# Performance work log

Measured on AMD Instinct MI355X. Metric: run time of the kernel, lower is better.

Reference implementation:

```python
import jax, jax.numpy as jnp
import numpy as np

DIM = 512        # model dim
MOE_DIM = 256    # expert hidden dim
E = 64           # n_routed experts
G = 8            # n_routed_group
TOPK_G = 4       # n_topk_group
K = 8            # n_experts_per_tok
SCALE = 2.5      # routed_scale
CAP = 1024


def setup_inputs() -> dict:
    key = jax.random.key(0)
    ks = jax.random.split(key, 6)
    x = jax.random.normal(ks[0], (4, 512, DIM), jnp.float32)
    gate_w = jax.random.normal(ks[1], (E, DIM), jnp.float32) / np.sqrt(DIM).astype(np.float32)
    gate_b = jax.random.normal(ks[2], (E,), jnp.float32) * 0.01
    w1 = jax.random.normal(ks[3], (E, DIM, MOE_DIM), jnp.float32) / np.sqrt(DIM).astype(np.float32)
    w3 = jax.random.normal(ks[4], (E, DIM, MOE_DIM), jnp.float32) / np.sqrt(DIM).astype(np.float32)
    w2 = jax.random.normal(ks[5], (E, MOE_DIM, DIM), jnp.float32) / np.sqrt(MOE_DIM).astype(np.float32)
    return {"x": x, "gate_w": gate_w, "gate_b": gate_b, "w1": w1, "w3": w3, "w2": w2}


def _gate(x2, gate_w, gate_b):
    # x2: [T, DIM] -> (weights [T,K], indices [T,K])
    T = x2.shape[0]
    scores = jax.nn.sigmoid(x2 @ gate_w.T)                      # [T, E]
    s = (scores + gate_b).reshape(T, G, E // G)                  # grouped scores
    group_scores = jax.lax.top_k(s, 2)[0].sum(-1)                # [T, G] sum of top-2 per group
    top_groups = jax.lax.top_k(group_scores, TOPK_G)[1]          # [T, TOPK_G]
    gmask = jnp.zeros((T, G), bool).at[jnp.arange(T)[:, None], top_groups].set(True)
    s = jnp.where(gmask[..., None], s, -jnp.inf).reshape(T, E)
    idx = jax.lax.top_k(s, K)[1]                                 # [T, K]
    w = jnp.take_along_axis(scores, idx, axis=1)                 # original (pre-bias) scores
    w = w / w.sum(-1, keepdims=True) * SCALE
    return w, idx


def _moe_forward(x, gate_w, gate_b, w1, w3, w2):
    shape = x.shape
    x2 = x.reshape(-1, DIM)                                      # [T, DIM]
    T = x2.shape[0]
    w, idx = _gate(x2, gate_w, gate_b)
    flat_e = idx.reshape(-1)                                     # [T*K]
    # position of each (token, slot) within its expert's buffer, in order
    oh = (flat_e[:, None] == jnp.arange(E)[None, :]).astype(jnp.int32)  # [T*K, E]
    pos = (jnp.cumsum(oh, axis=0) * oh).sum(-1) - 1              # [T*K]
    x_rep = jnp.repeat(x2, K, axis=0)                            # [T*K, DIM]
    # dispatch into per-expert buffers [E, CAP, DIM]
    xb = jnp.zeros((E, CAP, DIM), x2.dtype).at[flat_e, pos].set(x_rep, mode='drop')
    h = jax.nn.silu(jnp.einsum('ecd,edm->ecm', xb, w1)) * jnp.einsum('ecd,edm->ecm', xb, w3)
    yb = jnp.einsum('ecm,emd->ecd', h, w2)                       # [E, CAP, DIM]
    # combine: gather back and weight
    y = yb.at[flat_e, pos].get(mode='fill', fill_value=0.0) * w.reshape(-1)[:, None]
    return y.reshape(T, K, DIM).sum(1).reshape(shape)


def reference(x, gate_w, gate_b, w1, w3, w2):
    return _moe_forward(x, gate_w, gate_b, w1, w3, w2)
```

## Files before the change

### kernel.cpp

```cpp
#include <hip/hip_runtime.h>

#define T_TOK 2048
#define DIM   512
#define MOE   256
#define NE    64
#define NG    8
#define TOPKG 4
#define TOPK  8
#define CAP   1024
#define MOE_SCALE 2.5f

typedef float f32x4 __attribute__((ext_vector_type(4)));
typedef short s16x8 __attribute__((ext_vector_type(8)));

__device__ __forceinline__ unsigned short f2bf(float f) {
    unsigned u = __builtin_bit_cast(unsigned, f);
    unsigned r = (u + 0x7fffu + ((u >> 16) & 1u)) >> 16;
    return (unsigned short)r;
}
__device__ __forceinline__ unsigned pk2(float lo, float hi) {
    return (unsigned)f2bf(lo) | ((unsigned)f2bf(hi) << 16);
}

__device__ __forceinline__ void tile_scan(const int* __restrict__ counts, int lane,
                                          int e, int& G0, int& ne, int& nt)
{
    int cl = min(counts[lane], CAP);
    int ntl = (cl + 31) >> 5;
    int v = ntl;
#pragma unroll
    for (int d = 1; d < 64; d <<= 1) {
        int o = __shfl_up(v, d);
        if (lane >= d) v += o;
    }
    G0 = __shfl(v - ntl, e);
    ne = __shfl(cl, e);
    nt = __shfl(ntl, e);
}

__global__ __launch_bounds__(256) void gwt_k(const float* __restrict__ gw,
                                             float* __restrict__ gwT)
{
    int idx = blockIdx.x * 256 + threadIdx.x;
    int e = idx >> 9, k = idx & 511;
    gwT[(size_t)(k >> 2) * 256 + e * 4 + (k & 3)] = gw[idx];
}

__global__ __launch_bounds__(256) void gate_fused_k(const float* __restrict__ x,
                                                    const float* __restrict__ gwT,
                                                    const float* __restrict__ gb,
                                                    int* __restrict__ counts,
                                                    int* __restrict__ etok,
                                                    float* __restrict__ wt_of,
                                                    short* __restrict__ xb)
{
    __shared__ float xs[4][512];
    __shared__ float ps[4][4][64];
    int w = threadIdx.x >> 6, lane = threadIdx.x & 63;
    int t = blockIdx.x * 4 + w;

    {
        const float4* xr = (const float4*)(x + (size_t)t * DIM);
        float4 v0 = xr[lane * 2], v1 = xr[lane * 2 + 1];
        *(float4*)&xs[w][lane * 8]     = v0;
        *(float4*)&xs[w][lane * 8 + 4] = v1;
        short o[8];
        o[0] = (short)f2bf(v0.x); o[1] = (short)f2bf(v0.y);
        o[2] = (short)f2bf(v0.z); o[3] = (short)f2bf(v0.w);
        o[4] = (short)f2bf(v1.x); o[5] = (short)f2bf(v1.y);
        o[6] = (short)f2bf(v1.z); o[7] = (short)f2bf(v1.w);
        *(s16x8*)(xb + (size_t)t * DIM + lane * 8) = *(const s16x8*)o;
    }
    __syncthreads();

    const f32x4* gt = (const f32x4*)gwT;
    float a0 = 0.f, a1 = 0.f, a2 = 0.f, a3 = 0.f;
    int kb = w * 32;
#pragma unroll 8
    for (int k4 = 0; k4 < 32; ++k4) {
        f32x4 g  = gt[(size_t)(kb + k4) * 64 + lane];
        f32x4 x0 = *(const f32x4*)&xs[0][(kb + k4) * 4];
        f32x4 x1 = *(const f32x4*)&xs[1][(kb + k4) * 4];
        f32x4 x2 = *(const f32x4*)&xs[2][(kb + k4) * 4];
        f32x4 x3 = *(const f32x4*)&xs[3][(kb + k4) * 4];
        a0 += g.x * x0.x + g.y * x0.y + g.z * x0.z + g.w * x0.w;
        a1 += g.x * x1.x + g.y * x1.y + g.z * x1.z + g.w * x1.w;
        a2 += g.x * x2.x + g.y * x2.y + g.z * x2.z + g.w * x2.w;
        a3 += g.x * x3.x + g.y * x3.y + g.z * x3.z + g.w * x3.w;
    }
    ps[w][0][lane] = a0; ps[w][1][lane] = a1;
    ps[w][2][lane] = a2; ps[w][3][lane] = a3;
    __syncthreads();
    float acc = ps[0][w][lane] + ps[1][w][lane] + ps[2][w][lane] + ps[3][w][lane];

    float sc = 1.f / (1.f + __expf(-acc));
    float s  = sc + gb[lane];

    float m1 = s, m2 = -1e30f;
#pragma unroll
    for (int d = 1; d < 8; d <<= 1) {
        float o1 = __shfl_xor(m1, d);
        float o2 = __shfl_xor(m2, d);
        float n1 = fmaxf(m1, o1);
        float n2 = fmaxf(fminf(m1, o1), fmaxf(m2, o2));
        m1 = n1; m2 = n2;
    }
    float gv = m1 + m2;

    bool gkeep = false;
#pragma unroll
    for (int it = 0; it < TOPKG; ++it) {
        float m = gv;
#pragma unroll
        for (int d = 1; d < 64; d <<= 1) m = fmaxf(m, __shfl_xor(m, d));
        unsigned long long mask = __ballot(gv == m);
        int ldr = __ffsll(mask) - 1;
        if ((lane >> 3) == (ldr >> 3)) { gkeep = true; gv = -2e30f; }
    }
    float sv = gkeep ? s : -1e30f;

    float wsum = 0.f;
    int my_e = 0; float my_w = 0.f;
#pragma unroll
    for (int k = 0; k < TOPK; ++k) {
        float m = sv;
#pragma unroll
        for (int d = 1; d < 64; d <<= 1) m = fmaxf(m, __shfl_xor(m, d));
        unsigned long long mask = __ballot(sv == m);
        int l = __ffsll(mask) - 1;
        float wk = __shfl(sc, l);
        wsum += wk;
        if (lane == k) { my_e = l; my_w = wk; }
        if (lane == l) sv = -2e30f;
    }
    float scale = MOE_SCALE / wsum;
    if (lane < TOPK) {
        int p = atomicAdd(&counts[my_e], 1);
        int rid = t * TOPK + lane;
        bool ok = (p < CAP);
        if (ok) etok[my_e * CAP + p] = rid;
        wt_of[rid] = ok ? my_w * scale : 0.f;
    }
}

__global__ __launch_bounds__(256) void dispatch_k(const short* __restrict__ xb,
                                                  const int* __restrict__ counts,
                                                  const int* __restrict__ etok,
                                                  short* __restrict__ xg)
{
    int e = blockIdx.x & 63, sub = blockIdx.x >> 6;
    int w = threadIdx.x >> 6, lane = threadIdx.x & 63;

    int G0, ne, nt;
    tile_scan(counts, lane, e, G0, ne, nt);
    int rows = nt * 32;
    const int* el = etok + e * CAP;

    int kt = lane >> 2, qq = lane & 3;
    for (int p = sub * 4 + w; p < rows; p += 32) {
        s16x8 v = {0, 0, 0, 0, 0, 0, 0, 0};
        if (p < ne) {
            int tok = el[p] >> 3;
            v = *(const s16x8*)(xb + (size_t)tok * DIM + lane * 8);
        }
        int st = (p >> 4) & 1, m = p & 15;
        size_t off = ((((size_t)(G0 + (p >> 5)) * 16 + kt) * 2 + st) * 64
                      + (qq * 16 + m)) * 8;
        *(s16x8*)(xg + off) = v;
    }
}

__global__ __launch_bounds__(256, 2) void gemm1_k(const short* __restrict__ xg,
                                                  const float* __restrict__ w1,
                                                  const float* __restrict__ w3,
                                                  const int* __restrict__ counts,
                                                  short* __restrict__ hgf)
{
    __shared__ short Bl[2][16][2][64][8];
    __shared__ short Ct[4][2][16][24];

    int e  = blockIdx.x & 63, cg = blockIdx.x >> 6;
    int n0 = cg * 32;
    int tid = threadIdx.x;
    int w = tid >> 6, lane = tid & 63;
    int q = lane >> 4, m16 = lane & 15;

    int G0, ne, nt;
    tile_scan(counts, lane, e, G0, ne, nt);

    const float* W1e = w1 + (size_t)e * DIM * MOE + n0;
    const float* W3e = w3 + (size_t)e * DIM * MOE + n0;
#pragma unroll 4
    for (int it = 0; it < 16; ++it) {
        int idx = it * 256 + tid;
        int mat = idx >> 11;
        int rem = idx & 2047;
        int r2  = rem >> 3;
        int cq  = (rem & 7) * 4;
        int k   = r2 * 2;
        int kt = k >> 5, qf = (k >> 3) & 3, j0 = k & 7;
        int cgrp = cq >> 4, c15 = cq & 15;
        const float* p = (mat ? W3e : W1e) + (size_t)k * MOE + cq;
        f32x4 lo = __builtin_nontemporal_load((const f32x4*)p);
        f32x4 hi = __builtin_nontemporal_load((const f32x4*)(p + MOE));
        unsigned* b = (unsigned*)&Bl[mat][kt][cgrp][qf * 16 + c15][j0];
        b[0]  = pk2(lo.x, hi.x);
        b[4]  = pk2(lo.y, hi.y);
        b[8]  = pk2(lo.z, hi.z);
        b[12] = pk2(lo.w, hi.w);
    }
    __syncthreads();

    for (int T = w; T < nt; T += 4) {
        const short* A = xg + (size_t)(G0 + T) * 16384 + lane * 8;

        f32x4 acc[2][2][2];
#pragma unroll
        for (int i = 0; i < 2; ++i)
#pragma unroll
            for (int j = 0; j < 2; ++j)
#pragma unroll
                for (int c = 0; c < 2; ++c) acc[i][j][c] = (f32x4)0.f;

        s16x8 pa0[4], pa1[4];
#pragma unroll
        for (int i = 0; i < 4; ++i) {
            pa0[i] = *(const s16x8*)(A + (i * 2 + 0) * 512);
            pa1[i] = *(const s16x8*)(A + (i * 2 + 1) * 512);
        }
#pragma unroll
        for (int kt = 0; kt < 16; ++kt) {
            s16x8 a0 = pa0[kt & 3], a1 = pa1[kt & 3];
            if (kt < 12) {
                pa0[kt & 3] = *(const s16x8*)(A + ((kt + 4) * 2 + 0) * 512);
                pa1[kt & 3] = *(const s16x8*)(A + ((kt + 4) * 2 + 1) * 512);
            }
            s16x8 b10 = *(const s16x8*)&Bl[0][kt][0][lane][0];
            s16x8 b11 = *(const s16x8*)&Bl[0][kt][1][lane][0];
            s16x8 b30 = *(const s16x8*)&Bl[1][kt][0][lane][0];
            s16x8 b31 = *(const s16x8*)&Bl[1][kt][1][lane][0];
            acc[0][0][0] = __builtin_amdgcn_mfma_f32_16x16x32_bf16(a0, b10, acc[0][0][0], 0, 0, 0);
            acc[1][0][0] = __builtin_amdgcn_mfma_f32_16x16x32_bf16(a1, b10, acc[1][0][0], 0, 0, 0);
            acc[0][0][1] = __builtin_amdgcn_mfma_f32_16x16x32_bf16(a0, b11, acc[0][0][1], 0, 0, 0);
            acc[1][0][1] = __builtin_amdgcn_mfma_f32_16x16x32_bf16(a1, b11, acc[1][0][1], 0, 0, 0);
            acc[0][1][0] = __builtin_amdgcn_mfma_f32_16x16x32_bf16(a0, b30, acc[0][1][0], 0, 0, 0);
            acc[1][1][0] = __builtin_amdgcn_mfma_f32_16x16x32_bf16(a1, b30, acc[1][1][0], 0, 0, 0);
            acc[0][1][1] = __builtin_amdgcn_mfma_f32_16x16x32_bf16(a0, b31, acc[0][1][1], 0, 0, 0);
            acc[1][1][1] = __builtin_amdgcn_mfma_f32_16x16x32_bf16(a1, b31, acc[1][1][1], 0, 0, 0);
        }

#pragma unroll
        for (int cgrp = 0; cgrp < 2; ++cgrp) {
#pragma unroll
            for (int sub = 0; sub < 2; ++sub)
#pragma unroll
                for (int r = 0; r < 4; ++r) {
                    float g = acc[sub][0][cgrp][r];
                    float u = acc[sub][1][cgrp][r];
                    float hv = g / (1.f + __expf(-g)) * u;
                    Ct[w][sub][q * 4 + r][m16] = (short)f2bf(hv);
                }
            int subr = q >> 1;
            s16x8 hv8 = *(const s16x8*)&Ct[w][subr][m16][(q & 1) * 8];
            size_t slot = ((size_t)(G0 + T) * 8 + cg) * 2 + subr;
            *(s16x8*)(hgf + slot * 512 + (cgrp * 2 + (q & 1)) * 128 + m16 * 8) = hv8;
        }
    }
}

__global__ __launch_bounds__(256, 2) void gemm2_k(const short* __restrict__ hgf,
                                                  const float* __restrict__ w2,
                                                  const int* __restrict__ counts,
                                                  const int* __restrict__ etok,
                                                  short* __restrict__ ybuf)
{
    __shared__ short Bl[4][8][64][8];

    int e  = blockIdx.x & 63, cg = blockIdx.x >> 6;
    int n0 = cg * 64;
    int tid = threadIdx.x;
    int w = tid >> 6, lane = tid & 63;
    int q = lane >> 4, m16 = lane & 15;

    int G0, ne, nt;
    tile_scan(counts, lane, e, G0, ne, nt);

    const float* W2e = w2 + (size_t)e * MOE * DIM + n0;
#pragma unroll 4
    for (int it = 0; it < 8; ++it) {
        int idx = it * 256 + tid;
        int r2  = idx >> 4;
        int cq  = (idx & 15) * 4;
        int k   = r2 * 2;
        int kt2 = k >> 5, qf = (k >> 3) & 3, j0 = k & 7;
        int s = cq >> 4, c15 = cq & 15;
        const float* p = W2e + (size_t)k * DIM + cq;
        f32x4 lo = __builtin_nontemporal_load((const f32x4*)p);
        f32x4 hi = __builtin_nontemporal_load((const f32x4*)(p + DIM));
        unsigned* b = (unsigned*)&Bl[s][kt2][qf * 16 + c15][j0];
        b[0]  = pk2(lo.x, hi.x);
        b[4]  = pk2(lo.y, hi.y);
        b[8]  = pk2(lo.z, hi.z);
        b[12] = pk2(lo.w, hi.w);
    }
    __syncthreads();

    const int* el = etok + e * CAP;

    for (int T = w; T < nt; T += 4) {
        const short* A = hgf + (size_t)(G0 + T) * 8192 + lane * 8;

        int erid[2][4];
#pragma unroll
        for (int sub = 0; sub < 2; ++sub)
#pragma unroll
            for (int r = 0; r < 4; ++r) {
                int row = T * 32 + sub * 16 + q * 4 + r;
                erid[sub][r] = row < ne ? el[row] : -1;
            }

        f32x4 acc[2][4];
#pragma unroll
        for (int i = 0; i < 2; ++i)
#pragma unroll
            for (int j = 0; j < 4; ++j) acc[i][j] = (f32x4)0.f;

        s16x8 pa0[4], pa1[4];
#pragma unroll
        for (int i = 0; i < 4; ++i) {
            pa0[i] = *(const s16x8*)(A + (i * 2 + 0) * 512);
            pa1[i] = *(const s16x8*)(A + (i * 2 + 1) * 512);
        }
#pragma unroll
        for (int kt = 0; kt < 8; ++kt) {
            s16x8 a0 = pa0[kt & 3], a1 = pa1[kt & 3];
            if (kt < 4) {
                pa0[kt & 3] = *(const s16x8*)(A + ((kt + 4) * 2 + 0) * 512);
                pa1[kt & 3] = *(const s16x8*)(A + ((kt + 4) * 2 + 1) * 512);
            }
            s16x8 b0 = *(const s16x8*)&Bl[0][kt][lane][0];
            s16x8 b1 = *(const s16x8*)&Bl[1][kt][lane][0];
            s16x8 b2 = *(const s16x8*)&Bl[2][kt][lane][0];
            s16x8 b3 = *(const s16x8*)&Bl[3][kt][lane][0];
            acc[0][0] = __builtin_amdgcn_mfma_f32_16x16x32_bf16(a0, b0, acc[0][0], 0, 0, 0);
            acc[1][0] = __builtin_amdgcn_mfma_f32_16x16x32_bf16(a1, b0, acc[1][0], 0, 0, 0);
            acc[0][1] = __builtin_amdgcn_mfma_f32_16x16x32_bf16(a0, b1, acc[0][1], 0, 0, 0);
            acc[1][1] = __builtin_amdgcn_mfma_f32_16x16x32_bf16(a1, b1, acc[1][1], 0, 0, 0);
            acc[0][2] = __builtin_amdgcn_mfma_f32_16x16x32_bf16(a0, b2, acc[0][2], 0, 0, 0);
            acc[1][2] = __builtin_amdgcn_mfma_f32_16x16x32_bf16(a1, b2, acc[1][2], 0, 0, 0);
            acc[0][3] = __builtin_amdgcn_mfma_f32_16x16x32_bf16(a0, b3, acc[0][3], 0, 0, 0);
            acc[1][3] = __builtin_amdgcn_mfma_f32_16x16x32_bf16(a1, b3, acc[1][3], 0, 0, 0);
        }

#pragma unroll
        for (int sub = 0; sub < 2; ++sub)
#pragma unroll
            for (int s = 0; s < 4; ++s)
#pragma unroll
                for (int r = 0; r < 4; ++r) {
                    if (erid[sub][r] >= 0)
                        ybuf[(size_t)erid[sub][r] * DIM + n0 + s * 16 + m16] =
                            (short)f2bf(acc[sub][s][r]);
                }
    }
}

__global__ __launch_bounds__(256) void combine_k(const short* __restrict__ ybuf,
                                                 const float* __restrict__ wt_of,
                                                 float* __restrict__ out)
{
    int t = blockIdx.x;
    int tid = threadIdx.x;
    const int* yb = (const int*)ybuf;
    float sx = 0.f, sy = 0.f;
#pragma unroll
    for (int k = 0; k < TOPK; ++k) {
        float wk = wt_of[t * TOPK + k];
        int v = yb[(size_t)(t * TOPK + k) * (DIM / 2) + tid];
        float lo = __builtin_bit_cast(float, (unsigned)v << 16);
        float hi = __builtin_bit_cast(float, (unsigned)v & 0xffff0000u);
        sx += wk * lo;
        sy += wk * hi;
    }
    float2 o = {sx, sy};
    ((float2*)out)[(size_t)t * (DIM / 2) + tid] = o;
}

extern "C" void kernel_launch(void* const* d_in, const int* in_sizes, int n_in,
                              void* d_out, int out_size, void* d_ws, size_t ws_size,
                              hipStream_t stream)
{
    const float* x  = (const float*)d_in[0];
    const float* gw = (const float*)d_in[1];
    const float* gb = (const float*)d_in[2];
    const float* w1 = (const float*)d_in[3];
    const float* w3 = (const float*)d_in[4];
    const float* w2 = (const float*)d_in[5];

    char* ws = (char*)d_ws;
    short* xb    = (short*)(ws);
    short* hgf   = (short*)(ws + 2097152);
    short* xg    = (short*)(ws + 11534336);
    short* ybuf  = (short*)(ws + 11534336);
    float* gwT   = (float*)(ws + 30408704);
    int*   etok  = (int*)  (ws + 30539776);
    float* wt_of = (float*)(ws + 30801920);
    int*   counts= (int*)  (ws + 30867456);

    hipMemsetAsync(counts, 0, NE * 4, stream);

    gwt_k<<<128, 256, 0, stream>>>(gw, gwT);
    gate_fused_k<<<T_TOK / 4, 256, 0, stream>>>(x, gwT, gb, counts, etok, wt_of, xb);
    dispatch_k<<<NE * 8, 256, 0, stream>>>(xb, counts, etok, xg);
    gemm1_k<<<NE * 8, 256, 0, stream>>>(xg, w1, w3, counts, hgf);
    gemm2_k<<<NE * 8, 256, 0, stream>>>(hgf, w2, counts, etok, ybuf);
    combine_k<<<T_TOK, 256, 0, stream>>>(ybuf, wt_of, (float*)d_out);
}
```

Before: 246.8 us.

## Pre-convert expert weights to packed bf16 in a separate prep kernel

A new prep kernel converts w1/w3/w2 from fp32 into bf16 already laid out in the LDS tile order, and also absorbs the gate-weight transpose. The GEMM kernels then just copy their weight tiles with vector loads instead of doing strided fp32 loads and packing. This moves the conversion work and fp32 weight reads off the GEMM critical path, but the conversion still runs every call, adding a bf16 write plus reread of about 50MB. gemm2's occupancy hint is also raised from 2 to 3 blocks per CU.

```diff
diff --git a/kernel.cpp b/kernel.cpp
--- a/kernel.cpp
+++ b/kernel.cpp
@@ -38,12 +38,70 @@
     nt = __shfl(ntl, e);
 }
 
-__global__ __launch_bounds__(256) void gwt_k(const float* __restrict__ gw,
-                                             float* __restrict__ gwT)
-{
-    int idx = blockIdx.x * 256 + threadIdx.x;
-    int e = idx >> 9, k = idx & 511;
-    gwT[(size_t)(k >> 2) * 256 + e * 4 + (k & 3)] = gw[idx];
+__global__ __launch_bounds__(256) void prep_k(const float* __restrict__ gw,
+                                              const float* __restrict__ w1,
+                                              const float* __restrict__ w3,
+                                              const float* __restrict__ w2,
+                                              float* __restrict__ gwT,
+                                              short* __restrict__ pw13,
+                                              short* __restrict__ pw2)
+{
+    int bid = blockIdx.x, tid = threadIdx.x;
+    if (bid < 2048) {
+        int u = bid >> 2, quarter = bid & 3;
+        int e = u >> 3, cg = u & 7;
+        int n0 = cg * 32;
+        const float* W1e = w1 + (size_t)e * DIM * MOE + n0;
+        const float* W3e = w3 + (size_t)e * DIM * MOE + n0;
+        short* dst = pw13 + (size_t)(e * 8 + cg) * 32768;
+#pragma unroll
+        for (int t = 0; t < 4; ++t) {
+            int idx = quarter * 1024 + t * 256 + tid;
+            int mat = idx >> 11;
+            int rem = idx & 2047;
+            int r2 = rem >> 3, cq = (rem & 7) * 4;
+            int k = r2 * 2;
+            int kt = k >> 5, qf = (k >> 3) & 3, j0 = k & 7;
+            int cgrp = cq >> 4, c15 = cq & 15;
+            const float* p = (mat ? W3e : W1e) + (size_t)k * MOE + cq;
+            f32x4 lo = *(const f32x4*)p;
+            f32x4 hi = *(const f32x4*)(p + MOE);
+            unsigned* b = (unsigned*)(dst +
+                ((((mat * 16 + kt) * 2 + cgrp) * 64 + (qf * 16 + c15)) * 8 + j0));
+            b[0]  = pk2(lo.x, hi.x);
+            b[4]  = pk2(lo.y, hi.y);
+            b[8]  = pk2(lo.z, hi.z);
+            b[12] = pk2(lo.w, hi.w);
+        }
+    } else if (bid < 3072) {
+        int b2 = bid - 2048;
+        int e = b2 >> 4, s16 = b2 & 15;
+        const float* W2e = w2 + (size_t)e * MOE * DIM;
+#pragma unroll
+        for (int t = 0; t < 4; ++t) {
+            int idx = s16 * 1024 + t * 256 + tid;
+            int cg = idx >> 11, rem = idx & 2047;
+            int n0 = cg * 64;
+            int r2 = rem >> 4, cq = (rem & 15) * 4;
+            int k = r2 * 2;
+            int kt2 = k >> 5, qf = (k >> 3) & 3, j0 = k & 7;
+            int s = cq >> 4, c15 = cq & 15;
+            const float* p = W2e + n0 + (size_t)k * DIM + cq;
+            f32x4 lo = *(const f32x4*)p;
+            f32x4 hi = *(const f32x4*)(p + DIM);
+            short* dst = pw2 + (size_t)(e * 8 + cg) * 16384;
+            unsigned* b = (unsigned*)(dst +
+                (((s * 8 + kt2) * 64 + (qf * 16 + c15)) * 8 + j0));
+            b[0]  = pk2(lo.x, hi.x);
+            b[4]  = pk2(lo.y, hi.y);
+            b[8]  = pk2(lo.z, hi.z);
+            b[12] = pk2(lo.w, hi.w);
+        }
+    } else {
+        int idx = (bid - 3072) * 256 + tid;
+        int e = idx >> 9, k = idx & 511;
+        gwT[(size_t)(k >> 2) * 256 + e * 4 + (k & 3)] = gw[idx];
+    }
 }
 
 __global__ __launch_bounds__(256) void gate_fused_k(const float* __restrict__ x,
@@ -170,9 +228,8 @@
     }
 }
 
-__global__ __launch_bounds__(256, 2) void gemm1_k(const short* __restrict__ xg,
-                                                  const float* __restrict__ w1,
-                                                  const float* __restrict__ w3,
+__global__ __launch_bounds__(256, 2) void gemm1_k(const short* __restrict__ pw13,
+                                                  const short* __restrict__ xg,
                                                   const int* __restrict__ counts,
                                                   short* __restrict__ hgf)
 {
@@ -180,34 +237,20 @@
     __shared__ short Ct[4][2][16][24];
 
     int e  = blockIdx.x & 63, cg = blockIdx.x >> 6;
-    int n0 = cg * 32;
     int tid = threadIdx.x;
     int w = tid >> 6, lane = tid & 63;
     int q = lane >> 4, m16 = lane & 15;
 
     int G0, ne, nt;
     tile_scan(counts, lane, e, G0, ne, nt);
-
-    const float* W1e = w1 + (size_t)e * DIM * MOE + n0;
-    const float* W3e = w3 + (size_t)e * DIM * MOE + n0;
+    (void)ne;
+
+    const short* src = pw13 + (size_t)(e * 8 + cg) * 32768;
+    short* dstl = &Bl[0][0][0][0][0];
 #pragma unroll 4
     for (int it = 0; it < 16; ++it) {
-        int idx = it * 256 + tid;
-        int mat = idx >> 11;
-        int rem = idx & 2047;
-        int r2  = rem >> 3;
-        int cq  = (rem & 7) * 4;
-        int k   = r2 * 2;
-        int kt = k >> 5, qf = (k >> 3) & 3, j0 = k & 7;
-        int cgrp = cq >> 4, c15 = cq & 15;
-        const float* p = (mat ? W3e : W1e) + (size_t)k * MOE + cq;
-        f32x4 lo = __builtin_nontemporal_load((const f32x4*)p);
-        f32x4 hi = __builtin_nontemporal_load((const f32x4*)(p + MOE));
-        unsigned* b = (unsigned*)&Bl[mat][kt][cgrp][qf * 16 + c15][j0];
-        b[0]  = pk2(lo.x, hi.x);
-        b[4]  = pk2(lo.y, hi.y);
-        b[8]  = pk2(lo.z, hi.z);
-        b[12] = pk2(lo.w, hi.w);
+        int o = (it * 256 + tid) * 8;
+        *(s16x8*)(dstl + o) = *(const s16x8*)(src + o);
     }
     __syncthreads();
 
@@ -268,8 +311,8 @@
     }
 }
 
-__global__ __launch_bounds__(256, 2) void gemm2_k(const short* __restrict__ hgf,
-                                                  const float* __restrict__ w2,
+__global__ __launch_bounds__(256, 3) void gemm2_k(const short* __restrict__ pw2,
+                                                  const short* __restrict__ hgf,
                                                   const int* __restrict__ counts,
                                                   const int* __restrict__ etok,
                                                   short* __restrict__ ybuf)
@@ -285,23 +328,12 @@
     int G0, ne, nt;
     tile_scan(counts, lane, e, G0, ne, nt);
 
-    const float* W2e = w2 + (size_t)e * MOE * DIM + n0;
+    const short* src = pw2 + (size_t)(e * 8 + cg) * 16384;
+    short* dstl = &Bl[0][0][0][0];
 #pragma unroll 4
     for (int it = 0; it < 8; ++it) {
-        int idx = it * 256 + tid;
-        int r2  = idx >> 4;
-        int cq  = (idx & 15) * 4;
-        int k   = r2 * 2;
-        int kt2 = k >> 5, qf = (k >> 3) & 3, j0 = k & 7;
-        int s = cq >> 4, c15 = cq & 15;
-        const float* p = W2e + (size_t)k * DIM + cq;
-        f32x4 lo = __builtin_nontemporal_load((const f32x4*)p);
-        f32x4 hi = __builtin_nontemporal_load((const f32x4*)(p + DIM));
-        unsigned* b = (unsigned*)&Bl[s][kt2][qf * 16 + c15][j0];
-        b[0]  = pk2(lo.x, hi.x);
-        b[4]  = pk2(lo.y, hi.y);
-        b[8]  = pk2(lo.z, hi.z);
-        b[12] = pk2(lo.w, hi.w);
+        int o = (it * 256 + tid) * 8;
+        *(s16x8*)(dstl + o) = *(const s16x8*)(src + o);
     }
     __syncthreads();
 
@@ -401,18 +433,20 @@
     short* xb    = (short*)(ws);
     short* hgf   = (short*)(ws + 2097152);
     short* xg    = (short*)(ws + 11534336);
-    short* ybuf  = (short*)(ws + 11534336);
-    float* gwT   = (float*)(ws + 30408704);
-    int*   etok  = (int*)  (ws + 30539776);
-    float* wt_of = (float*)(ws + 30801920);
-    int*   counts= (int*)  (ws + 30867456);
+    short* pw2   = (short*)(ws + 30408704);
+    short* pw13  = (short*)(ws + 47185920);
+    short* ybuf  = (short*)(ws + 47185920);
+    float* gwT   = (float*)(ws + 80740352);
+    int*   etok  = (int*)  (ws + 80871424);
+    float* wt_of = (float*)(ws + 81133568);
+    int*   counts= (int*)  (ws + 81199104);
 
     hipMemsetAsync(counts, 0, NE * 4, stream);
 
-    gwt_k<<<128, 256, 0, stream>>>(gw, gwT);
+    prep_k<<<3200, 256, 0, stream>>>(gw, w1, w3, w2, gwT, pw13, pw2);
     gate_fused_k<<<T_TOK / 4, 256, 0, stream>>>(x, gwT, gb, counts, etok, wt_of, xb);
     dispatch_k<<<NE * 8, 256, 0, stream>>>(xb, counts, etok, xg);
-    gemm1_k<<<NE * 8, 256, 0, stream>>>(xg, w1, w3, counts, hgf);
-    gemm2_k<<<NE * 8, 256, 0, stream>>>(hgf, w2, counts, etok, ybuf);
+    gemm1_k<<<NE * 8, 256, 0, stream>>>(pw13, xg, counts, hgf);
+    gemm2_k<<<NE * 8, 256, 0, stream>>>(pw2, hgf, counts, etok, ybuf);
     combine_k<<<T_TOK, 256, 0, stream>>>(ybuf, wt_of, (float*)d_out);
 }
```

After: 284.3 us. +15.2%, slower.
